# Performance work log

Hardware: AMD Instinct MI355X
Metric: run time of the kernel (lower is better)

The kernel has to match this reference:

```python
import jax, jax.numpy as jnp
import numpy as np

N = 33554432
MARGIN = 1.0


def setup_inputs() -> dict:
    key = jax.random.key(0)
    k1, k2 = jax.random.split(key)
    predictions = jax.random.normal(k1, (N,), dtype=jnp.float32)
    # labels in {-1, +1}
    labels = 2 * jax.random.randint(k2, (N,), 0, 2, dtype=jnp.int32) - 1
    return {"predictions": predictions, "labels": labels}


def reference(predictions, labels):
    # Original loop math:
    #   over positives: a += 1; b += 2*(margin - p_i); c += (margin - p_i)^2
    #   over negatives: loss += a*p_j^2 + b*p_j + c
    # Vectorized as masked reductions.
    dt = predictions.dtype
    pos = labels == 1
    neg = labels == -1
    z = jnp.where(pos, MARGIN - predictions, jnp.zeros((), dt))  # margin - p on positives
    a = jnp.sum(pos.astype(dt))
    b = 2.0 * jnp.sum(z)
    c = jnp.sum(z * z)
    pn = jnp.where(neg, predictions, jnp.zeros((), dt))
    n_neg = jnp.sum(neg.astype(dt))
    loss = a * jnp.sum(pn * pn) + b * jnp.sum(pn) + c * n_neg
    return loss
```

## Files before the change

kernel.cpp:

```cpp
#include <hip/hip_runtime.h>


constexpr float MARGIN = 1.0f;

#define BANK_STRIDE 32
#define BLOCK 256
#define WAVES 4
#define SLOTS 4
#define GROUPS_PER_BLOCK (BLOCK * SLOTS)

#define GLOBAL_AS __attribute__((address_space(1)))
#define LDS_AS    __attribute__((address_space(3)))

__device__ __forceinline__ float wave_reduce(float v) {
    #pragma unroll
    for (int off = 32; off > 0; off >>= 1) v += __shfl_down(v, off, 64);
    return v;
}

__global__ __launch_bounds__(BLOCK) void hinge2_reduce(
    const float* __restrict__ pred, const int* __restrict__ lab,
    float* __restrict__ ws, int nvec, int nbanks, int bank_stride)
{
    const float4* p4 = reinterpret_cast<const float4*>(pred);
    const int4*   l4 = reinterpret_cast<const int4*>(lab);

    __shared__ float4 sp_[WAVES][SLOTS][64];
    __shared__ int4   sl_[WAVES][SLOTS][64];

    float a = 0.f, sz = 0.f, sz2 = 0.f, sp = 0.f, sp2 = 0.f;

    #define ACC(px, lx) do {                         \
        float ispos = ((lx) == 1) ? 1.0f : 0.0f;     \
        float z  = ispos * (MARGIN - (px));          \
        a   += ispos;                                \
        sz  += z;                                    \
        sz2 += z * z;                                \
        float pn = ((lx) == 1) ? 0.0f : (px);        \
        sp  += pn;                                   \
        sp2 += pn * pn;                              \
    } while (0)
    #define ACC4(p, l) do {                          \
        ACC((p).x, (l).x); ACC((p).y, (l).y);        \
        ACC((p).z, (l).z); ACC((p).w, (l).w);        \
    } while (0)

    const int lane = threadIdx.x & 63;
    const int wid  = threadIdx.x >> 6;
    const int blockBase = blockIdx.x * GROUPS_PER_BLOCK;

    if (blockBase + GROUPS_PER_BLOCK <= nvec) {
        #pragma unroll
        for (int s = 0; s < SLOTS; ++s) {
            int g = blockBase + wid * (SLOTS * 64) + s * 64 + lane;
            __builtin_amdgcn_global_load_lds(
                (const GLOBAL_AS void*)(p4 + g),
                (LDS_AS void*)&sp_[wid][s][0], 16, 0, 0);
        }
        #pragma unroll
        for (int s = 0; s < SLOTS; ++s) {
            int g = blockBase + wid * (SLOTS * 64) + s * 64 + lane;
            __builtin_amdgcn_global_load_lds(
                (const GLOBAL_AS void*)(l4 + g),
                (LDS_AS void*)&sl_[wid][s][0], 16, 0, 0);
        }
        __syncthreads();

        #pragma unroll
        for (int s = 0; s < SLOTS; ++s) {
            float4 p = sp_[wid][s][lane];
            int4   l = sl_[wid][s][lane];
            ACC4(p, l);
        }
    } else {
        for (int s = 0; s < SLOTS; ++s) {
            int g = blockBase + wid * (SLOTS * 64) + s * 64 + lane;
            if (g < nvec) {
                float4 p = p4[g];
                int4   l = l4[g];
                ACC4(p, l);
            }
        }
    }
    #undef ACC4
    #undef ACC

    a   = wave_reduce(a);
    sz  = wave_reduce(sz);
    sz2 = wave_reduce(sz2);
    sp  = wave_reduce(sp);
    sp2 = wave_reduce(sp2);

    __shared__ float sdata[WAVES][5];
    if (lane == 0) {
        sdata[wid][0] = a;
        sdata[wid][1] = sz;
        sdata[wid][2] = sz2;
        sdata[wid][3] = sp;
        sdata[wid][4] = sp2;
    }
    __syncthreads();

    if (threadIdx.x == 0) {
        float t0 = 0.f, t1 = 0.f, t2 = 0.f, t3 = 0.f, t4 = 0.f;
        #pragma unroll
        for (int w = 0; w < WAVES; ++w) {
            t0 += sdata[w][0];
            t1 += sdata[w][1];
            t2 += sdata[w][2];
            t3 += sdata[w][3];
            t4 += sdata[w][4];
        }
        float* bank = ws + (blockIdx.x & (nbanks - 1)) * bank_stride;
        atomicAdd(&bank[0], t0);
        atomicAdd(&bank[1], t1);
        atomicAdd(&bank[2], t2);
        atomicAdd(&bank[3], t3);
        atomicAdd(&bank[4], t4);
    }
}

__global__ __launch_bounds__(256) void hinge2_final(
    const float* __restrict__ ws,
    const float* __restrict__ pred, const int* __restrict__ lab,
    float* __restrict__ out, int n, int tail_start,
    int nbanks, int bank_stride)
{
    int t = threadIdx.x;
    float a = 0.f, sz = 0.f, sz2 = 0.f, sp = 0.f, sp2 = 0.f;
    for (int b = t; b < nbanks; b += 256) {
        const float* bank = ws + b * bank_stride;
        a   += bank[0];
        sz  += bank[1];
        sz2 += bank[2];
        sp  += bank[3];
        sp2 += bank[4];
    }
    a   = wave_reduce(a);
    sz  = wave_reduce(sz);
    sz2 = wave_reduce(sz2);
    sp  = wave_reduce(sp);
    sp2 = wave_reduce(sp2);

    __shared__ float sdata[4][5];
    int lane = t & 63, wid = t >> 6;
    if (lane == 0) {
        sdata[wid][0] = a;  sdata[wid][1] = sz; sdata[wid][2] = sz2;
        sdata[wid][3] = sp; sdata[wid][4] = sp2;
    }
    __syncthreads();

    if (t == 0) {
        double A = 0, SZ = 0, SZ2 = 0, SP = 0, SP2 = 0;
        #pragma unroll
        for (int w = 0; w < 4; ++w) {
            A   += sdata[w][0];
            SZ  += sdata[w][1];
            SZ2 += sdata[w][2];
            SP  += sdata[w][3];
            SP2 += sdata[w][4];
        }
        for (int i = tail_start; i < n; ++i) {
            float p = pred[i];
            if (lab[i] == 1) {
                double z = (double)MARGIN - (double)p;
                A += 1.0; SZ += z; SZ2 += z * z;
            } else {
                SP += (double)p; SP2 += (double)p * (double)p;
            }
        }
        double loss = A * SP2 + 2.0 * SZ * SP + SZ2 * ((double)n - A);
        out[0] = (float)loss;
    }
}

extern "C" void kernel_launch(void* const* d_in, const int* in_sizes, int n_in,
                              void* d_out, int out_size, void* d_ws, size_t ws_size,
                              hipStream_t stream)
{
    const float* pred = (const float*)d_in[0];
    const int*   lab  = (const int*)d_in[1];
    float*       out  = (float*)d_out;
    float*       ws   = (float*)d_ws;

    int n    = in_sizes[0];
    int nvec = n >> 2;
    int tail = nvec << 2;

    int bank_stride = BANK_STRIDE;
    size_t max_banks = ws_size / (bank_stride * sizeof(float));
    int nbanks = 1;
    if (max_banks == 0) { bank_stride = 5; nbanks = 1; }
    else { while (nbanks * 2 <= (int)max_banks && nbanks < 256) nbanks <<= 1; }

    hipMemsetAsync(ws, 0, (size_t)nbanks * bank_stride * sizeof(float), stream);

    int blocks = (nvec + GROUPS_PER_BLOCK - 1) / GROUPS_PER_BLOCK;
    if (blocks < 1) blocks = 1;
    hinge2_reduce<<<blocks, BLOCK, 0, stream>>>(pred, lab, ws, nvec, nbanks, bank_stride);
    hinge2_final<<<1, BLOCK, 0, stream>>>(ws, pred, lab, out, n, tail, nbanks, bank_stride);
}
```

Before: 276.1 us.

## Software-pipeline per-wave LDS loads with a ring buffer and vmcnt waits

Each wave now streams 16 chunks through a 4-slot LDS ring buffer. Loads are issued three chunks ahead, and explicit s_waitcnt vmcnt counts replace the block-wide __syncthreads, so memory traffic overlaps with accumulation. Each block now covers four times as many elements, which means fewer blocks and fewer atomic bank updates. The risk is lower occupancy and a reliance on hand-counted vmcnt values; a slot is also overwritten right after it is read.

Result: no change. 279.4 us (+1.2%).

```diff
diff --git a/kernel.cpp b/kernel.cpp
--- a/kernel.cpp
+++ b/kernel.cpp
@@ -7,7 +7,10 @@
 #define BLOCK 256
 #define WAVES 4
 #define SLOTS 4
-#define GROUPS_PER_BLOCK (BLOCK * SLOTS)
+#define CPW 16
+#define CHUNK 64
+#define GROUPS_PER_WAVE (CPW * CHUNK)
+#define GROUPS_PER_BLOCK (WAVES * GROUPS_PER_WAVE)
 
 #define GLOBAL_AS __attribute__((address_space(1)))
 #define LDS_AS    __attribute__((address_space(3)))
@@ -25,8 +28,8 @@
     const float4* p4 = reinterpret_cast<const float4*>(pred);
     const int4*   l4 = reinterpret_cast<const int4*>(lab);
 
-    __shared__ float4 sp_[WAVES][SLOTS][64];
-    __shared__ int4   sl_[WAVES][SLOTS][64];
+    __shared__ float4 spred[WAVES][SLOTS][CHUNK];
+    __shared__ int4   slab [WAVES][SLOTS][CHUNK];
 
     float a = 0.f, sz = 0.f, sz2 = 0.f, sp = 0.f, sp2 = 0.f;
 
@@ -45,36 +48,36 @@
         ACC((p).z, (l).z); ACC((p).w, (l).w);        \
     } while (0)
 
-    const int lane = threadIdx.x & 63;
-    const int wid  = threadIdx.x >> 6;
-    const int blockBase = blockIdx.x * GROUPS_PER_BLOCK;
-
-    if (blockBase + GROUPS_PER_BLOCK <= nvec) {
+    const int lane  = threadIdx.x & 63;
+    const int wid   = threadIdx.x >> 6;
+    const int gbase = (blockIdx.x * WAVES + wid) * GROUPS_PER_WAVE;
+
+    #define ISSUE(c) do {                                                     \
+        int gg = gbase + (c) * CHUNK + lane;                                  \
+        __builtin_amdgcn_global_load_lds(                                     \
+            (const GLOBAL_AS void*)(p4 + gg),                                 \
+            (LDS_AS void*)&spred[wid][(c) & (SLOTS - 1)][0], 16, 0, 0);       \
+        __builtin_amdgcn_global_load_lds(                                     \
+            (const GLOBAL_AS void*)(l4 + gg),                                 \
+            (LDS_AS void*)&slab [wid][(c) & (SLOTS - 1)][0], 16, 0, 0);       \
+    } while (0)
+
+    if (gbase + GROUPS_PER_WAVE <= nvec) {
+        ISSUE(0); ISSUE(1); ISSUE(2);
         #pragma unroll
-        for (int s = 0; s < SLOTS; ++s) {
-            int g = blockBase + wid * (SLOTS * 64) + s * 64 + lane;
-            __builtin_amdgcn_global_load_lds(
-                (const GLOBAL_AS void*)(p4 + g),
-                (LDS_AS void*)&sp_[wid][s][0], 16, 0, 0);
-        }
-        #pragma unroll
-        for (int s = 0; s < SLOTS; ++s) {
-            int g = blockBase + wid * (SLOTS * 64) + s * 64 + lane;
-            __builtin_amdgcn_global_load_lds(
-                (const GLOBAL_AS void*)(l4 + g),
-                (LDS_AS void*)&sl_[wid][s][0], 16, 0, 0);
-        }
-        __syncthreads();
-
-        #pragma unroll
-        for (int s = 0; s < SLOTS; ++s) {
-            float4 p = sp_[wid][s][lane];
-            int4   l = sl_[wid][s][lane];
+        for (int k = 0; k < CPW; ++k) {
+            if (k + 3 < CPW) ISSUE(k + 3);
+            if      (k <  CPW - 3) asm volatile("s_waitcnt vmcnt(6)" ::: "memory");
+            else if (k == CPW - 3) asm volatile("s_waitcnt vmcnt(4)" ::: "memory");
+            else if (k == CPW - 2) asm volatile("s_waitcnt vmcnt(2)" ::: "memory");
+            else                   asm volatile("s_waitcnt vmcnt(0)" ::: "memory");
+            float4 p = spred[wid][k & (SLOTS - 1)][lane];
+            int4   l = slab [wid][k & (SLOTS - 1)][lane];
             ACC4(p, l);
         }
     } else {
-        for (int s = 0; s < SLOTS; ++s) {
-            int g = blockBase + wid * (SLOTS * 64) + s * 64 + lane;
+        for (int c = 0; c < CPW; ++c) {
+            int g = gbase + c * CHUNK + lane;
             if (g < nvec) {
                 float4 p = p4[g];
                 int4   l = l4[g];
@@ -82,6 +85,7 @@
             }
         }
     }
+    #undef ISSUE
     #undef ACC4
     #undef ACC
 
```
